# Kernel tuning notes

Measured on AMD Instinct MI355X. Metric: run time of the kernel, lower is better.

## Reference

```python
import jax, jax.numpy as jnp
import numpy as np
import math

IMG_CHL = 1024
L_CHL = 512
N_PTS = 4096  # pinned by nn.LayerNorm(4096)
H = 256
W = 256
HEADS = 4
VOXEL = 1.0 / 256.0
PC_MIN = 0.0
BEV_STRIDE = 1.0
LN_EPS = 1e-5


def setup_inputs() -> dict:
    key = jax.random.key(0)
    ks = jax.random.split(key, 6)
    point_features = jax.random.normal(ks[0], (1, L_CHL, N_PTS), jnp.float32)
    kp = jax.random.uniform(ks[1], (N_PTS, 4), dtype=jnp.float32)
    keypoints = kp.at[:, 0].set(0.0)  # batch index column = 0 (batch_size=1)
    bev_features = jax.random.normal(ks[2], (1, IMG_CHL, H, W), jnp.float32)
    conv_L_w = jax.random.normal(ks[3], (L_CHL, L_CHL), jnp.float32) * 0.02
    conv_L_b = jnp.zeros((L_CHL,), jnp.float32)
    img_head_w = jax.random.normal(ks[4], (HEADS, L_CHL, IMG_CHL), jnp.float32) * 0.02
    img_head_b = jnp.zeros((HEADS, L_CHL), jnp.float32)
    ln_w = jnp.ones((N_PTS,), jnp.float32)
    ln_b = jnp.zeros((N_PTS,), jnp.float32)
    conv_fusion_w = jax.random.normal(ks[5], (L_CHL, L_CHL), jnp.float32) * 0.02
    conv_fusion_b = jnp.zeros((L_CHL,), jnp.float32)
    return {
        "point_features": point_features,
        "keypoints": keypoints,
        "bev_features": bev_features,
        "conv_L_w": conv_L_w,
        "conv_L_b": conv_L_b,
        "img_head_w": img_head_w,
        "img_head_b": img_head_b,
        "ln_w": ln_w,
        "ln_b": ln_b,
        "conv_fusion_w": conv_fusion_w,
        "conv_fusion_b": conv_fusion_b,
    }


def _bilinear_interpolate(im, x, y):
    """im: (H, W, C); x, y: (N,). Mirrors bilinear_interpolate_torch (clamped corners)."""
    x0 = jnp.clip(jnp.floor(x).astype(jnp.int32), 0, im.shape[1] - 1)
    x1 = jnp.clip(jnp.floor(x).astype(jnp.int32) + 1, 0, im.shape[1] - 1)
    y0 = jnp.clip(jnp.floor(y).astype(jnp.int32), 0, im.shape[0] - 1)
    y1 = jnp.clip(jnp.floor(y).astype(jnp.int32) + 1, 0, im.shape[0] - 1)
    Ia = im[y0, x0]  # (N, C)
    Ib = im[y1, x0]
    Ic = im[y0, x1]
    Id = im[y1, x1]
    x0f, x1f = x0.astype(x.dtype), x1.astype(x.dtype)
    y0f, y1f = y0.astype(y.dtype), y1.astype(y.dtype)
    wa = (x1f - x) * (y1f - y)
    wb = (x1f - x) * (y - y0f)
    wc = (x - x0f) * (y1f - y)
    wd = (x - x0f) * (y - y0f)
    return Ia * wa[:, None] + Ib * wb[:, None] + Ic * wc[:, None] + Id * wd[:, None]


def reference(point_features, keypoints, bev_features, conv_L_w, conv_L_b,
              img_head_w, img_head_b, ln_w, ln_b, conv_fusion_w, conv_fusion_b):
    # --- interpolate_from_bev_features (batch_size=1, all keypoints in batch 0) ---
    x_idxs = (keypoints[:, 1] - PC_MIN) / VOXEL / BEV_STRIDE
    y_idxs = (keypoints[:, 2] - PC_MIN) / VOXEL / BEV_STRIDE
    im = jnp.transpose(bev_features[0], (1, 2, 0))  # (H, W, C)
    point_bev = _bilinear_interpolate(im, x_idxs, y_idxs)  # (N, IMG_CHL)
    img_features = point_bev.T[None]  # (1, IMG_CHL, N)

    # --- Fusion_Conv_att ---
    # 1x1 Conv1d == channel matmul
    L_query = jnp.einsum('oc,bcn->bon', conv_L_w, point_features) + conv_L_b[None, :, None]  # (1, L, N)
    keys = jnp.einsum('hoc,bcn->hbon', img_head_w, img_features) + img_head_b[:, None, :, None]  # (4, 1, L, N)
    dk = L_CHL
    score = jnp.sum(keys * L_query[None], axis=2)[:, 0, :] / math.sqrt(dk)  # (4, N)
    weightmap = jax.nn.softmax(score, axis=0)[None]  # (1, 4, N) softmax over heads
    z = jnp.einsum('hn,hln->ln', weightmap[0], keys[:, 0])[None]  # (1, L, N)

    t = z + L_query
    mu = jnp.mean(t, axis=-1, keepdims=True)
    var = jnp.mean((t - mu) ** 2, axis=-1, keepdims=True)
    t = (t - mu) / jnp.sqrt(var + LN_EPS) * ln_w + ln_b  # LayerNorm over the 4096 point axis

    fusion_features = jnp.einsum('oc,bcn->bon', conv_fusion_w, t) + conv_fusion_b[None, :, None]
    return fusion_features, weightmap
```

## Files before the change

kernel.cpp:

```cpp
#include <hip/hip_runtime.h>

typedef unsigned short u16;
typedef unsigned int   u32;

typedef short s16x8 __attribute__((ext_vector_type(8)));
typedef float f32x4 __attribute__((ext_vector_type(4)));

__device__ __forceinline__ float b2f(u16 u) {
    u32 x = ((u32)u) << 16;
    float f;
    __builtin_memcpy(&f, &x, 4);
    return f;
}

__device__ __forceinline__ u16 f2b(float f) {
    u32 x;
    __builtin_memcpy(&x, &f, 4);
    u32 r = (x + 0x7fffu + ((x >> 16) & 1u)) >> 16;
    return (u16)r;
}

__device__ __forceinline__ void gload_lds16(const u16* g, u16* l) {
    __builtin_amdgcn_global_load_lds(
        (const __attribute__((address_space(1))) void*)g,
        (__attribute__((address_space(3))) void*)l, 16, 0, 0);
}

__global__ void prep_points(const float* __restrict__ kp,
                            int4* __restrict__ pts_off,
                            float4* __restrict__ pts_w,
                            int* __restrict__ perm) {
    __shared__ int cnt[256];
    __shared__ int base[256];
    const int t = threadIdx.x;
    cnt[t] = 0;
    __syncthreads();
    int buck[16];
    #pragma unroll
    for (int j = 0; j < 16; j++) {
        const int n = j * 256 + t;
        const float x = kp[n * 4 + 1] * 256.0f;
        const float y = kp[n * 4 + 2] * 256.0f;
        const int x0 = min(max((int)floorf(x), 0), 255);
        const int y0 = min(max((int)floorf(y), 0), 255);
        const int b = (y0 >> 3) * 8 + (x0 >> 5);
        buck[j] = b;
        atomicAdd(&cnt[b], 1);
    }
    __syncthreads();
    if (t < 64) {
        int a0 = cnt[t * 4], a1 = cnt[t * 4 + 1], a2 = cnt[t * 4 + 2], a3 = cnt[t * 4 + 3];
        int tot = a0 + a1 + a2 + a3;
        int pre = tot;
        #pragma unroll
        for (int off = 1; off < 64; off <<= 1) {
            int v = __shfl_up(pre, off);
            if (t >= off) pre += v;
        }
        int excl = pre - tot;
        base[t * 4]     = excl;
        base[t * 4 + 1] = excl + a0;
        base[t * 4 + 2] = excl + a0 + a1;
        base[t * 4 + 3] = excl + a0 + a1 + a2;
    }
    __syncthreads();
    cnt[t] = 0;
    __syncthreads();
    #pragma unroll
    for (int j = 0; j < 16; j++) {
        const int n = j * 256 + t;
        const float x = kp[n * 4 + 1] * 256.0f;
        const float y = kp[n * 4 + 2] * 256.0f;
        const float xf = floorf(x), yf = floorf(y);
        const int x0 = min(max((int)xf, 0), 255);
        const int x1 = min(max((int)xf + 1, 0), 255);
        const int y0 = min(max((int)yf, 0), 255);
        const int y1 = min(max((int)yf + 1, 0), 255);
        const float x0f = (float)x0, x1f = (float)x1;
        const float y0f = (float)y0, y1f = (float)y1;
        float4 w;
        w.x = (x1f - x) * (y1f - y);
        w.y = (x1f - x) * (y - y0f);
        w.z = (x - x0f) * (y1f - y);
        w.w = (x - x0f) * (y - y0f);
        int4 o;
        o.x = y0 * 256 + x0;
        o.y = y1 * 256 + x0;
        o.z = y0 * 256 + x1;
        o.w = y1 * 256 + x1;
        const int b = buck[j];
        const int pos = base[b] + atomicAdd(&cnt[b], 1);
        perm[pos] = n;
        pts_off[pos] = o;
        pts_w[pos] = w;
    }
}

__global__ __launch_bounds__(256) void interp_sorted(const float* __restrict__ bev,
                                                     const int4* __restrict__ pts_off,
                                                     const float4* __restrict__ pts_w,
                                                     u16* __restrict__ img) {
    const int c = blockIdx.x;
    const float* plane = bev + (size_t)c * 65536;
    const int base_i = blockIdx.y * 1024;
    const int t = threadIdx.x;
    #pragma unroll
    for (int j = 0; j < 4; j++) {
        const int i = base_i + j * 256 + t;
        const int4 o = pts_off[i];
        const float4 w = pts_w[i];
        const float v = plane[o.x] * w.x + plane[o.y] * w.y +
                        plane[o.z] * w.z + plane[o.w] * w.w;
        img[(size_t)c * 4096 + i] = f2b(v);
    }
}

__global__ void convert_params(const float* clw, const float* ihw, const float* cfw,
                               const float* clb, const float* ihb,
                               const float* lnw, const float* lnb, const float* cfb,
                               u16* __restrict__ canon) {
    const int total = 2632704;
    for (int i = blockIdx.x * 256 + threadIdx.x; i < total; i += gridDim.x * 256) {
        const float* src; int off;
        if (i < 262144)       { src = clw; off = i; }
        else if (i < 2359296) { src = ihw; off = i - 262144; }
        else if (i < 2621440) { src = cfw; off = i - 2359296; }
        else if (i < 2621952) { src = clb; off = i - 2621440; }
        else if (i < 2624000) { src = ihb; off = i - 2621952; }
        else if (i < 2628096) { src = lnw; off = i - 2624000; }
        else if (i < 2632192) { src = lnb; off = i - 2628096; }
        else                  { src = cfb; off = i - 2632192; }
        canon[i] = f2b(src[off]);
    }
}

template <int ISF>
__global__ void transpose_any(const void* __restrict__ in, u16* __restrict__ out,
                              int R, int C, const int* __restrict__ perm) {
    __shared__ u16 tile[64][65];
    const int t = threadIdx.x;
    const int r0 = blockIdx.y * 64, c0 = blockIdx.x * 64;
    #pragma unroll
    for (int i = 0; i < 16; i++) {
        int idx = i * 256 + t;
        int r = idx >> 6, c = idx & 63;
        tile[r][c] = ISF ? f2b(((const float*)in)[(size_t)(r0 + r) * C + c0 + c])
                         : ((const u16*)in)[(size_t)(r0 + r) * C + c0 + c];
    }
    __syncthreads();
    #pragma unroll
    for (int i = 0; i < 16; i++) {
        int idx = i * 256 + t;
        int c = idx >> 6, r = idx & 63;
        int row = perm ? perm[c0 + c] : (c0 + c);
        out[(size_t)row * R + r0 + r] = tile[r][c];
    }
}

template <int BM, int OB>
__global__ __launch_bounds__(256) void gemm_bt(const u16* __restrict__ A,
                                               const u16* __restrict__ BT,
                                               const u16* __restrict__ bias,
                                               void* __restrict__ Cout,
                                               int M, int N, int K) {
    constexpr int MT = BM / 32;
    __shared__ __align__(16) u16 As[BM * 32];
    __shared__ __align__(16) u16 Bs[128 * 32];
    const int tid = threadIdx.x;
    const int lane = tid & 63;
    const int w = tid >> 6;
    const int m0 = blockIdx.y * BM;
    const int n0 = blockIdx.x * 128;
    const int wm = (w >> 1) * (BM / 2);
    const int wn = (w & 1) * 64;

    f32x4 acc[MT][4] = {};

    const int q = lane >> 4, r = lane & 15;

    for (int k0 = 0; k0 < K; k0 += 32) {
        __syncthreads();
        #pragma unroll
        for (int i = 0; i < BM / 64; i++) {
            int s = i * 256 + tid;
            gload_lds16(&A[(size_t)(m0 + (s >> 2)) * K + k0 + (s & 3) * 8], &As[s * 8]);
        }
        #pragma unroll
        for (int i = 0; i < 2; i++) {
            int s = i * 256 + tid;
            gload_lds16(&BT[(size_t)(n0 + (s >> 2)) * K + k0 + (s & 3) * 8], &Bs[s * 8]);
        }
        __syncthreads();

        s16x8 af[MT], bfr[4];
        #pragma unroll
        for (int mt = 0; mt < MT; mt++)
            af[mt] = *(const s16x8*)&As[(wm + mt * 16 + r) * 32 + q * 8];
        #pragma unroll
        for (int nt = 0; nt < 4; nt++)
            bfr[nt] = *(const s16x8*)&Bs[(wn + nt * 16 + r) * 32 + q * 8];
        #pragma unroll
        for (int mt = 0; mt < MT; mt++)
            #pragma unroll
            for (int nt = 0; nt < 4; nt++)
                acc[mt][nt] = __builtin_amdgcn_mfma_f32_16x16x32_bf16(
                    af[mt], bfr[nt], acc[mt][nt], 0, 0, 0);
    }

    const int cn = lane & 15;
    #pragma unroll
    for (int mt = 0; mt < MT; mt++) {
        #pragma unroll
        for (int i = 0; i < 4; i++) {
            int gm = m0 + wm + mt * 16 + q * 4 + i;
            float bv = b2f(bias[gm]);
            #pragma unroll
            for (int nt = 0; nt < 4; nt++) {
                int gn = n0 + wn + nt * 16 + cn;
                float v = acc[mt][nt][i] + bv;
                if (OB)
                    ((u16*)Cout)[(size_t)gm * N + gn] = f2b(v);
                else
                    ((float*)Cout)[(size_t)gm * N + gn] = v;
            }
        }
    }
}

__global__ void score_partial(const u16* __restrict__ keys,
                              const float* __restrict__ lq,
                              float* __restrict__ spart) {
    __shared__ float red[4][4][64];
    const int nl = threadIdx.x & 63;
    const int ls = threadIdx.x >> 6;
    const int n = blockIdx.x * 64 + nl;
    const int lbase = blockIdx.y * 128 + ls * 32;
    float acc[4] = {0.f, 0.f, 0.f, 0.f};
    #pragma unroll 8
    for (int i = 0; i < 32; i++) {
        const int l = lbase + i;
        const float qv = lq[l * 4096 + n];
        #pragma unroll
        for (int h = 0; h < 4; h++)
            acc[h] += b2f(keys[(size_t)(h * 512 + l) * 4096 + n]) * qv;
    }
    #pragma unroll
    for (int h = 0; h < 4; h++) red[h][ls][nl] = acc[h];
    __syncthreads();
    if (threadIdx.x < 64) {
        #pragma unroll
        for (int h = 0; h < 4; h++) {
            float s = red[h][0][nl] + red[h][1][nl] + red[h][2][nl] + red[h][3][nl];
            spart[(size_t)(blockIdx.y * 4 + h) * 4096 + n] = s;
        }
    }
}

__global__ void score_finalize(const float* __restrict__ spart,
                               float* __restrict__ wm_ws,
                               float* __restrict__ out) {
    const int n = blockIdx.x * 256 + threadIdx.x;
    const float scale = 0.044194173824159216f;
    float s[4];
    #pragma unroll
    for (int h = 0; h < 4; h++) {
        float v = 0.f;
        #pragma unroll
        for (int lc = 0; lc < 4; lc++) v += spart[(size_t)(lc * 4 + h) * 4096 + n];
        s[h] = v * scale;
    }
    float mx = fmaxf(fmaxf(s[0], s[1]), fmaxf(s[2], s[3]));
    float e[4], sum = 0.f;
    #pragma unroll
    for (int h = 0; h < 4; h++) { e[h] = expf(s[h] - mx); sum += e[h]; }
    const float inv = 1.0f / sum;
    #pragma unroll
    for (int h = 0; h < 4; h++) {
        float wv = e[h] * inv;
        wm_ws[h * 4096 + n] = wv;
        out[2097152 + (size_t)h * 4096 + n] = wv;
    }
}

__global__ __launch_bounds__(256) void compute_t_ln(const u16* __restrict__ keys,
                                                    const float* __restrict__ lq,
                                                    const float* __restrict__ wm_ws,
                                                    const float* __restrict__ lnw,
                                                    const float* __restrict__ lnb,
                                                    u16* __restrict__ tnorm) {
    const int l = blockIdx.x;
    const int t = threadIdx.x;
    float tv[16];
    float s = 0.f, ss = 0.f;
    #pragma unroll
    for (int j = 0; j < 16; j++) {
        const int n = j * 256 + t;
        float v = lq[l * 4096 + n];
        #pragma unroll
        for (int h = 0; h < 4; h++)
            v += wm_ws[h * 4096 + n] * b2f(keys[(size_t)(h * 512 + l) * 4096 + n]);
        tv[j] = v;
        s += v;
        ss += v * v;
    }
    for (int off = 32; off > 0; off >>= 1) {
        s += __shfl_down(s, off);
        ss += __shfl_down(ss, off);
    }
    __shared__ float bs[4], bss[4];
    const int w = t >> 6, lane = t & 63;
    if (lane == 0) { bs[w] = s; bss[w] = ss; }
    __syncthreads();
    const float S = bs[0] + bs[1] + bs[2] + bs[3];
    const float SS = bss[0] + bss[1] + bss[2] + bss[3];
    const float mu = S * (1.0f / 4096.0f);
    const float rstd = rsqrtf(SS * (1.0f / 4096.0f) - mu * mu + 1e-5f);
    #pragma unroll
    for (int j = 0; j < 16; j++) {
        const int n = j * 256 + t;
        const float v = (tv[j] - mu) * rstd * lnw[n] + lnb[n];
        tnorm[(size_t)l * 4096 + n] = f2b(v);
    }
}

extern "C" void kernel_launch(void* const* d_in, const int* in_sizes, int n_in,
                              void* d_out, int out_size, void* d_ws, size_t ws_size,
                              hipStream_t stream) {
    const float* pf  = (const float*)d_in[0];
    const float* kp  = (const float*)d_in[1];
    const float* bev = (const float*)d_in[2];
    const float* clw = (const float*)d_in[3];
    const float* clb = (const float*)d_in[4];
    const float* ihw = (const float*)d_in[5];
    const float* ihb = (const float*)d_in[6];
    const float* lnw = (const float*)d_in[7];
    const float* lnb = (const float*)d_in[8];
    const float* cfw = (const float*)d_in[9];
    const float* cfb = (const float*)d_in[10];
    float* out = (float*)d_out;

    char* ws = (char*)d_ws;
    u16*    img     = (u16*)(ws + 0);
    u16*    tnorm   = (u16*)(ws + 0);
    u16*    imgT    = (u16*)(ws + (8ull << 20));
    float*  lq      = (float*)(ws + (8ull << 20));
    u16*    keys    = (u16*)(ws + (16ull << 20));
    u16*    pfT     = (u16*)(ws + (32ull << 20));
    u16*    tT      = (u16*)(ws + (32ull << 20));
    float*  spart   = (float*)(ws + (36ull << 20));
    float*  wm_ws   = (float*)(ws + (36ull << 20) + 262144);
    u16*    canon   = (u16*)  (ws + (36ull << 20) + 332864);
    int4*   pts_off = (int4*) (ws + (42ull << 20));
    float4* pts_w   = (float4*)(ws + (42ull << 20) + 65536);
    int*    perm    = (int*)  (ws + (42ull << 20) + 131072);

    u16* clw_c = canon;
    u16* ihw_c = canon + 262144;
    u16* cfw_c = canon + 2359296;
    u16* clb_c = canon + 2621440;
    u16* ihb_c = canon + 2621952;
    u16* cfb_c = canon + 2632192;

    prep_points<<<1, 256, 0, stream>>>(kp, pts_off, pts_w, perm);
    convert_params<<<1024, 256, 0, stream>>>(clw, ihw, cfw, clb, ihb, lnw, lnb, cfb, canon);
    interp_sorted<<<dim3(1024, 4), 256, 0, stream>>>(bev, pts_off, pts_w, img);
    transpose_any<0><<<dim3(64, 16), 256, 0, stream>>>(img, imgT, 1024, 4096, perm);
    transpose_any<1><<<dim3(64, 8), 256, 0, stream>>>(pf, pfT, 512, 4096, nullptr);
    gemm_bt<128, 1><<<dim3(32, 16), 256, 0, stream>>>(ihw_c, imgT, ihb_c, keys, 2048, 4096, 1024);
    gemm_bt<64, 0><<<dim3(32, 8), 256, 0, stream>>>(clw_c, pfT, clb_c, lq, 512, 4096, 512);
    score_partial<<<dim3(64, 4), 256, 0, stream>>>(keys, lq, spart);
    score_finalize<<<16, 256, 0, stream>>>(spart, wm_ws, out);
    compute_t_ln<<<512, 256, 0, stream>>>(keys, lq, wm_ws, lnw, lnb, tnorm);
    transpose_any<0><<<dim3(64, 8), 256, 0, stream>>>(tnorm, tT, 512, 4096, nullptr);
    gemm_bt<64, 0><<<dim3(32, 8), 256, 0, stream>>>(cfw_c, tT, cfb_c, out, 512, 4096, 512);
}
```

Before: 518.0 us.

## Merge small launches and add larger pipelined 128x256 GEMM for keys projection

Folds point bucketing into the parameter conversion launch, merges the two input transposes into one launch, and fuses score partial reduction with softmax into one kernel. Replaces the keys-projection GEMM with a 512-thread, 128x256-tile kernel using a 4-stage LDS ring with global_load_lds prefetch, XOR swizzling, block swizzle and setprio. The aim is to cut launch overhead and improve MFMA utilisation on the largest GEMM. The trade-offs are fewer blocks (256) for that GEMM and a score kernel with only 64 blocks, which lowers parallelism there.

```diff
diff --git a/kernel.cpp b/kernel.cpp
--- a/kernel.cpp
+++ b/kernel.cpp
@@ -26,10 +26,31 @@
         (__attribute__((address_space(3))) void*)l, 16, 0, 0);
 }
 
-__global__ void prep_points(const float* __restrict__ kp,
-                            int4* __restrict__ pts_off,
-                            float4* __restrict__ pts_w,
-                            int* __restrict__ perm) {
+__global__ void prep_convert(const float* __restrict__ kp,
+                             int4* __restrict__ pts_off,
+                             float4* __restrict__ pts_w,
+                             int* __restrict__ perm,
+                             const float* clw, const float* ihw, const float* cfw,
+                             const float* clb, const float* ihb,
+                             const float* lnw, const float* lnb, const float* cfb,
+                             u16* __restrict__ canon) {
+    if (blockIdx.x != 0) {
+        const int total = 2632704;
+        const int stride = (gridDim.x - 1) * 256;
+        for (int i = (blockIdx.x - 1) * 256 + threadIdx.x; i < total; i += stride) {
+            const float* src; int off;
+            if (i < 262144)       { src = clw; off = i; }
+            else if (i < 2359296) { src = ihw; off = i - 262144; }
+            else if (i < 2621440) { src = cfw; off = i - 2359296; }
+            else if (i < 2621952) { src = clb; off = i - 2621440; }
+            else if (i < 2624000) { src = ihb; off = i - 2621952; }
+            else if (i < 2628096) { src = lnw; off = i - 2624000; }
+            else if (i < 2632192) { src = lnb; off = i - 2628096; }
+            else                  { src = cfb; off = i - 2632192; }
+            canon[i] = f2b(src[off]);
+        }
+        return;
+    }
     __shared__ int cnt[256];
     __shared__ int base[256];
     const int t = threadIdx.x;
@@ -115,28 +136,37 @@
     }
 }
 
-__global__ void convert_params(const float* clw, const float* ihw, const float* cfw,
-                               const float* clb, const float* ihb,
-                               const float* lnw, const float* lnb, const float* cfb,
-                               u16* __restrict__ canon) {
-    const int total = 2632704;
-    for (int i = blockIdx.x * 256 + threadIdx.x; i < total; i += gridDim.x * 256) {
-        const float* src; int off;
-        if (i < 262144)       { src = clw; off = i; }
-        else if (i < 2359296) { src = ihw; off = i - 262144; }
-        else if (i < 2621440) { src = cfw; off = i - 2359296; }
-        else if (i < 2621952) { src = clb; off = i - 2621440; }
-        else if (i < 2624000) { src = ihb; off = i - 2621952; }
-        else if (i < 2628096) { src = lnw; off = i - 2624000; }
-        else if (i < 2632192) { src = lnb; off = i - 2628096; }
-        else                  { src = cfb; off = i - 2632192; }
-        canon[i] = f2b(src[off]);
-    }
-}
-
-template <int ISF>
-__global__ void transpose_any(const void* __restrict__ in, u16* __restrict__ out,
-                              int R, int C, const int* __restrict__ perm) {
+__global__ void transpose_both(const u16* __restrict__ img, const float* __restrict__ pf,
+                               u16* __restrict__ imgT, u16* __restrict__ pfT,
+                               const int* __restrict__ perm) {
+    __shared__ u16 tile[64][65];
+    const int t = threadIdx.x;
+    int by = blockIdx.y;
+    int isf, R;
+    const int* prm;
+    u16* out;
+    if (by < 16) { isf = 0; R = 1024; prm = perm; out = imgT; }
+    else         { isf = 1; R = 512;  prm = nullptr; out = pfT; by -= 16; }
+    const int r0 = by * 64, c0 = blockIdx.x * 64;
+    #pragma unroll
+    for (int i = 0; i < 16; i++) {
+        int idx = i * 256 + t;
+        int r = idx >> 6, c = idx & 63;
+        tile[r][c] = isf ? f2b(pf[(size_t)(r0 + r) * 4096 + c0 + c])
+                         : img[(size_t)(r0 + r) * 4096 + c0 + c];
+    }
+    __syncthreads();
+    #pragma unroll
+    for (int i = 0; i < 16; i++) {
+        int idx = i * 256 + t;
+        int c = idx >> 6, r = idx & 63;
+        int row = prm ? prm[c0 + c] : (c0 + c);
+        out[(size_t)row * R + r0 + r] = tile[r][c];
+    }
+}
+
+__global__ void transpose_u16(const u16* __restrict__ in, u16* __restrict__ out,
+                              int R, int C) {
     __shared__ u16 tile[64][65];
     const int t = threadIdx.x;
     const int r0 = blockIdx.y * 64, c0 = blockIdx.x * 64;
@@ -144,16 +174,106 @@
     for (int i = 0; i < 16; i++) {
         int idx = i * 256 + t;
         int r = idx >> 6, c = idx & 63;
-        tile[r][c] = ISF ? f2b(((const float*)in)[(size_t)(r0 + r) * C + c0 + c])
-                         : ((const u16*)in)[(size_t)(r0 + r) * C + c0 + c];
+        tile[r][c] = in[(size_t)(r0 + r) * C + c0 + c];
     }
     __syncthreads();
     #pragma unroll
     for (int i = 0; i < 16; i++) {
         int idx = i * 256 + t;
         int c = idx >> 6, r = idx & 63;
-        int row = perm ? perm[c0 + c] : (c0 + c);
-        out[(size_t)row * R + r0 + r] = tile[r][c];
+        out[(size_t)(c0 + c) * R + r0 + r] = tile[r][c];
+    }
+}
+
+__global__ __launch_bounds__(512, 1) void gemm_k256(const u16* __restrict__ A,
+                                                    const u16* __restrict__ BT,
+                                                    const u16* __restrict__ bias,
+                                                    u16* __restrict__ Cout,
+                                                    int M, int N, int K) {
+    __shared__ __align__(16) u16 As[4][128 * 32];
+    __shared__ __align__(16) u16 Bs[4][256 * 32];
+    const int tid = threadIdx.x;
+    const int lane = tid & 63;
+    const int w = tid >> 6;
+    const int bid = blockIdx.x;
+    const int swz = (bid & 7) * 32 + (bid >> 3);
+    const int m0 = (swz >> 4) * 128;
+    const int n0 = (swz & 15) * 256;
+    const int wm = (w >> 2) * 64;
+    const int wn = (w & 3) * 64;
+    const int q = lane >> 4, r = lane & 15;
+
+    const int ra = tid >> 2;
+    const int ka = ((tid & 3) ^ (ra & 3)) * 8;
+    const int rb0 = tid >> 2;
+    const int kb0 = ((tid & 3) ^ (rb0 & 3)) * 8;
+    const int sb1 = 512 + tid;
+    const int rb1 = sb1 >> 2;
+    const int kb1 = ((sb1 & 3) ^ (rb1 & 3)) * 8;
+
+    const int nkt = K >> 5;
+    f32x4 acc[4][4] = {};
+
+    {
+        gload_lds16(&A[(size_t)(m0 + ra) * K + ka], &As[0][tid * 8]);
+        gload_lds16(&BT[(size_t)(n0 + rb0) * K + kb0], &Bs[0][tid * 8]);
+        gload_lds16(&BT[(size_t)(n0 + rb1) * K + kb1], &Bs[0][sb1 * 8]);
+        gload_lds16(&A[(size_t)(m0 + ra) * K + 32 + ka], &As[1][tid * 8]);
+        gload_lds16(&BT[(size_t)(n0 + rb0) * K + 32 + kb0], &Bs[1][tid * 8]);
+        gload_lds16(&BT[(size_t)(n0 + rb1) * K + 32 + kb1], &Bs[1][sb1 * 8]);
+        asm volatile("s_waitcnt vmcnt(3)" ::: "memory");
+        __builtin_amdgcn_s_barrier();
+    }
+
+    for (int kt = 0; kt < nkt; kt++) {
+        const int b = kt & 3;
+        const u16* Ab = As[b];
+        const u16* Bb = Bs[b];
+        s16x8 af[4], bf[4];
+        #pragma unroll
+        for (int mt = 0; mt < 4; mt++) {
+            const int row = wm + mt * 16 + r;
+            af[mt] = *(const s16x8*)&Ab[row * 32 + ((q ^ (row & 3)) * 8)];
+        }
+        #pragma unroll
+        for (int nt = 0; nt < 4; nt++) {
+            const int row = wn + nt * 16 + r;
+            bf[nt] = *(const s16x8*)&Bb[row * 32 + ((q ^ (row & 3)) * 8)];
+        }
+        if (kt + 2 < nkt) {
+            const int b2 = (kt + 2) & 3;
+            const int k2 = (kt + 2) * 32;
+            gload_lds16(&A[(size_t)(m0 + ra) * K + k2 + ka], &As[b2][tid * 8]);
+            gload_lds16(&BT[(size_t)(n0 + rb0) * K + k2 + kb0], &Bs[b2][tid * 8]);
+            gload_lds16(&BT[(size_t)(n0 + rb1) * K + k2 + kb1], &Bs[b2][sb1 * 8]);
+        }
+        __builtin_amdgcn_s_barrier();
+        __builtin_amdgcn_s_setprio(1);
+        #pragma unroll
+        for (int mt = 0; mt < 4; mt++)
+            #pragma unroll
+            for (int nt = 0; nt < 4; nt++)
+                acc[mt][nt] = __builtin_amdgcn_mfma_f32_16x16x32_bf16(
+                    af[mt], bf[nt], acc[mt][nt], 0, 0, 0);
+        __builtin_amdgcn_s_setprio(0);
+        if (kt + 2 < nkt) asm volatile("s_waitcnt vmcnt(3)" ::: "memory");
+        else              asm volatile("s_waitcnt vmcnt(0)" ::: "memory");
+        __builtin_amdgcn_s_barrier();
+    }
+
+    const int cn = lane & 15;
+    #pragma unroll
+    for (int mt = 0; mt < 4; mt++) {
+        #pragma unroll
+        for (int i = 0; i < 4; i++) {
+            const int gm = m0 + wm + mt * 16 + q * 4 + i;
+            const float bv = b2f(bias[gm]);
+            #pragma unroll
+            for (int nt = 0; nt < 4; nt++) {
+                const int gn = n0 + wn + nt * 16 + cn;
+                Cout[(size_t)gm * N + gn] = f2b(acc[mt][nt][i] + bv);
+            }
+        }
     }
 }
 
@@ -227,18 +347,18 @@
     }
 }
 
-__global__ void score_partial(const u16* __restrict__ keys,
-                              const float* __restrict__ lq,
-                              float* __restrict__ spart) {
-    __shared__ float red[4][4][64];
+__global__ __launch_bounds__(512) void score_softmax(const u16* __restrict__ keys,
+                                                     const float* __restrict__ lq,
+                                                     float* __restrict__ wm_ws,
+                                                     float* __restrict__ out) {
+    __shared__ float red[4][8][64];
     const int nl = threadIdx.x & 63;
     const int ls = threadIdx.x >> 6;
     const int n = blockIdx.x * 64 + nl;
-    const int lbase = blockIdx.y * 128 + ls * 32;
     float acc[4] = {0.f, 0.f, 0.f, 0.f};
     #pragma unroll 8
-    for (int i = 0; i < 32; i++) {
-        const int l = lbase + i;
+    for (int i = 0; i < 64; i++) {
+        const int l = ls * 64 + i;
         const float qv = lq[l * 4096 + n];
         #pragma unroll
         for (int h = 0; h < 4; h++)
@@ -248,37 +368,26 @@
     for (int h = 0; h < 4; h++) red[h][ls][nl] = acc[h];
     __syncthreads();
     if (threadIdx.x < 64) {
+        const float scale = 0.044194173824159216f;
+        float s[4];
         #pragma unroll
         for (int h = 0; h < 4; h++) {
-            float s = red[h][0][nl] + red[h][1][nl] + red[h][2][nl] + red[h][3][nl];
-            spart[(size_t)(blockIdx.y * 4 + h) * 4096 + n] = s;
-        }
-    }
-}
-
-__global__ void score_finalize(const float* __restrict__ spart,
-                               float* __restrict__ wm_ws,
-                               float* __restrict__ out) {
-    const int n = blockIdx.x * 256 + threadIdx.x;
-    const float scale = 0.044194173824159216f;
-    float s[4];
-    #pragma unroll
-    for (int h = 0; h < 4; h++) {
-        float v = 0.f;
-        #pragma unroll
-        for (int lc = 0; lc < 4; lc++) v += spart[(size_t)(lc * 4 + h) * 4096 + n];
-        s[h] = v * scale;
-    }
-    float mx = fmaxf(fmaxf(s[0], s[1]), fmaxf(s[2], s[3]));
-    float e[4], sum = 0.f;
-    #pragma unroll
-    for (int h = 0; h < 4; h++) { e[h] = expf(s[h] - mx); sum += e[h]; }
-    const float inv = 1.0f / sum;
-    #pragma unroll
-    for (int h = 0; h < 4; h++) {
-        float wv = e[h] * inv;
-        wm_ws[h * 4096 + n] = wv;
-        out[2097152 + (size_t)h * 4096 + n] = wv;
+            float v = 0.f;
+            #pragma unroll
+            for (int c = 0; c < 8; c++) v += red[h][c][nl];
+            s[h] = v * scale;
+        }
+        float mx = fmaxf(fmaxf(s[0], s[1]), fmaxf(s[2], s[3]));
+        float e[4], sum = 0.f;
+        #pragma unroll
+        for (int h = 0; h < 4; h++) { e[h] = expf(s[h] - mx); sum += e[h]; }
+        const float inv = 1.0f / sum;
+        #pragma unroll
+        for (int h = 0; h < 4; h++) {
+            float wv = e[h] * inv;
+            wm_ws[h * 4096 + n] = wv;
+            out[2097152 + (size_t)h * 4096 + n] = wv;
+        }
     }
 }
 
@@ -347,9 +456,8 @@
     u16*    keys    = (u16*)(ws + (16ull << 20));
     u16*    pfT     = (u16*)(ws + (32ull << 20));
     u16*    tT      = (u16*)(ws + (32ull << 20));
-    float*  spart   = (float*)(ws + (36ull << 20));
-    float*  wm_ws   = (float*)(ws + (36ull << 20) + 262144);
-    u16*    canon   = (u16*)  (ws + (36ull << 20) + 332864);
+    float*  wm_ws   = (float*)(ws + (36ull << 20));
+    u16*    canon   = (u16*)  (ws + (36ull << 20) + 131072);
     int4*   pts_off = (int4*) (ws + (42ull << 20));
     float4* pts_w   = (float4*)(ws + (42ull << 20) + 65536);
     int*    perm    = (int*)  (ws + (42ull << 20) + 131072);
@@ -361,16 +469,14 @@
     u16* ihb_c = canon + 2621952;
     u16* cfb_c = canon + 2632192;
 
-    prep_points<<<1, 256, 0, stream>>>(kp, pts_off, pts_w, perm);
-    convert_params<<<1024, 256, 0, stream>>>(clw, ihw, cfw, clb, ihb, lnw, lnb, cfb, canon);
+    prep_convert<<<1025, 256, 0, stream>>>(kp, pts_off, pts_w, perm,
+                                           clw, ihw, cfw, clb, ihb, lnw, lnb, cfb, canon);
     interp_sorted<<<dim3(1024, 4), 256, 0, stream>>>(bev, pts_off, pts_w, img);
-    transpose_any<0><<<dim3(64, 16), 256, 0, stream>>>(img, imgT, 1024, 4096, perm);
-    transpose_any<1><<<dim3(64, 8), 256, 0, stream>>>(pf, pfT, 512, 4096, nullptr);
-    gemm_bt<128, 1><<<dim3(32, 16), 256, 0, stream>>>(ihw_c, imgT, ihb_c, keys, 2048, 4096, 1024);
+    transpose_both<<<dim3(64, 24), 256, 0, stream>>>(img, pf, imgT, pfT, perm);
+    gemm_k256<<<256, 512, 0, stream>>>(ihw_c, imgT, ihb_c, keys, 2048, 4096, 1024);
     gemm_bt<64, 0><<<dim3(32, 8), 256, 0, stream>>>(clw_c, pfT, clb_c, lq, 512, 4096, 512);
-    score_partial<<<dim3(64, 4), 256, 0, stream>>>(keys, lq, spart);
-    score_finalize<<<16, 256, 0, stream>>>(spart, wm_ws, out);
+    score_softmax<<<64, 512, 0, stream>>>(keys, lq, wm_ws, out);
     compute_t_ln<<<512, 256, 0, stream>>>(keys, lq, wm_ws, lnw, lnb, tnorm);
-    transpose_any<0><<<dim3(64, 8), 256, 0, stream>>>(tnorm, tT, 512, 4096, nullptr);
+    transpose_u16<<<dim3(64, 8), 256, 0, stream>>>(tnorm, tT, 512, 4096);
     gemm_bt<64, 0><<<dim3(32, 8), 256, 0, stream>>>(cfw_c, tT, cfb_c, out, 512, 4096, 512);
 }
```

Result: faster. 491.5 us (-5.1%).
